# Optimization experiments

Measured on AMD Instinct MI355X. Metric: run time of the kernel, lower is better.

## Reference

```python
import jax, jax.numpy as jnp
import numpy as np

TAU, LBDA, THETA = 0.25, 0.15, 0.3
N_WARPS, N_ITERS = 1, 30
EPS = 1e-12  # GRAD_IS_ZERO

GAUSS = jnp.array([
    [0.000874, 0.006976, 0.01386, 0.006976, 0.000874],
    [0.006976, 0.0557, 0.110656, 0.0557, 0.006976],
    [0.01386, 0.110656, 0.219833, 0.110656, 0.01386],
    [0.006976, 0.0557, 0.110656, 0.0557, 0.006976],
    [0.000874, 0.006976, 0.01386, 0.006976, 0.000874]], dtype=jnp.float32)


def to_gray(x):  # [B,3,H,W] -> [B,1,H,W], BGR-style weights from repo
    w = jnp.array([0.114, 0.587, 0.299], x.dtype)
    return jnp.einsum('bchw,c->bhw', x, w)[:, None]


def normalize_pair(x1, x2):
    mn = jnp.minimum(x1.min(), x2.min())
    mx = jnp.maximum(x1.max(), x2.max())
    den = mx - mn
    return 255.0 * (x1 - mn) / den, 255.0 * (x2 - mn) / den


def gaussian_smooth(x):
    k = GAUSS[None, None].astype(x.dtype)
    return jax.lax.conv_general_dilated(x, k, (1, 1), 'SAME')


def centered_grad(x):  # central differences, one-sided at borders (scaled 0.5)
    dx = jnp.concatenate([0.5 * (x[..., 1:2] - x[..., 0:1]),
                          0.5 * (x[..., 2:] - x[..., :-2]),
                          0.5 * (x[..., -1:] - x[..., -2:-1])], axis=-1)
    dy = jnp.concatenate([0.5 * (x[..., 1:2, :] - x[..., 0:1, :]),
                          0.5 * (x[..., 2:, :] - x[..., :-2, :]),
                          0.5 * (x[..., -1:, :] - x[..., -2:-1, :])], axis=-2)
    return dx, dy


def fwd_grad(x):  # forward differences, zero at last col/row
    dx = jnp.concatenate([x[..., 1:] - x[..., :-1], jnp.zeros_like(x[..., :1])], axis=-1)
    dy = jnp.concatenate([x[..., 1:, :] - x[..., :-1, :], jnp.zeros_like(x[..., :1, :])], axis=-2)
    return dx, dy


def divergence(px, py):  # adjoint of fwd_grad (backward differences with boundary handling)
    xp = jnp.concatenate([jnp.zeros_like(px[..., :1]), px[..., :-1]], axis=-1)
    yp = jnp.concatenate([jnp.zeros_like(py[..., :1, :]), py[..., :-1, :]], axis=-2)
    dx = jnp.concatenate([xp[..., 1:] - xp[..., :-1], -xp[..., -1:]], axis=-1)
    dy = jnp.concatenate([yp[..., 1:, :] - yp[..., :-1, :], -yp[..., -1:, :]], axis=-2)
    return dx + dy


def warp(x, u, v):  # grid_sample bilinear, align_corners=True, zeros padding
    B, C, H, W = x.shape
    base_x = jnp.linspace(-1.0, 1.0, W)[None, None, :]
    base_y = jnp.linspace(-1.0, 1.0, H)[None, :, None]
    gx = base_x + 2.0 * u[:, 0] / W   # [B,H,W]
    gy = base_y + 2.0 * v[:, 0] / H
    ix = (gx + 1.0) * 0.5 * (W - 1)
    iy = (gy + 1.0) * 0.5 * (H - 1)
    ix0 = jnp.floor(ix); iy0 = jnp.floor(iy)
    wx = ix - ix0; wy = iy - iy0

    def gather(yy, xx):
        valid = (xx >= 0) & (xx <= W - 1) & (yy >= 0) & (yy <= H - 1)
        xi = jnp.clip(xx, 0, W - 1).astype(jnp.int32)
        yi = jnp.clip(yy, 0, H - 1).astype(jnp.int32)
        flat = (yi * W + xi).reshape(B, 1, H * W)
        g = jnp.take_along_axis(x.reshape(B, C, H * W), flat, axis=2).reshape(B, C, H, W)
        return g * valid[:, None].astype(x.dtype)

    return (gather(iy0, ix0) * ((1 - wx) * (1 - wy))[:, None]
            + gather(iy0, ix0 + 1) * (wx * (1 - wy))[:, None]
            + gather(iy0 + 1, ix0) * ((1 - wx) * wy)[:, None]
            + gather(iy0 + 1, ix0 + 1) * (wx * wy)[:, None])


def tvnet_scale(x1, x2, u1, u2):
    l_t = LBDA * THETA
    taut = TAU / THETA
    d2x, d2y = centered_grad(x2)
    p11 = jnp.zeros_like(x1); p12 = jnp.zeros_like(x1)
    p21 = jnp.zeros_like(x1); p22 = jnp.zeros_like(x1)
    rho = jnp.zeros_like(x1)
    for _ in range(N_WARPS):
        x2w = warp(x2, u1, u2)
        dxw = warp(d2x, u1, u2)
        dyw = warp(d2y, u1, u2)
        grad = dxw ** 2 + dyw ** 2 + EPS
        rho_c = x2w - dxw * u1 - dyw * u2 - x1

        def body(carry, _):
            u1, u2, p11, p12, p21, p22, _ = carry
            rho = rho_c + dxw * u1 + dyw * u2 + EPS
            th = l_t * grad
            m3 = (rho >= -th) & (rho <= th) & (grad > EPS)
            coef = (jnp.where(rho < -th, l_t, 0.0)
                    + jnp.where(rho > th, -l_t, 0.0)
                    + jnp.where(m3, -rho / grad, 0.0))
            v1 = coef * dxw + u1
            v2 = coef * dyw + u2
            u1n = v1 + THETA * divergence(p11, p12)
            u2n = v2 + THETA * divergence(p21, p22)
            u1x, u1y = fwd_grad(u1n)
            u2x, u2y = fwd_grad(u2n)
            ng1 = 1.0 + taut * jnp.sqrt(u1x ** 2 + u1y ** 2 + EPS)
            ng2 = 1.0 + taut * jnp.sqrt(u2x ** 2 + u2y ** 2 + EPS)
            p11n = (p11 + taut * u1x) / ng1
            p12n = (p12 + taut * u1y) / ng1
            p21n = (p21 + taut * u2x) / ng2
            p22n = (p22 + taut * u2y) / ng2
            return (u1n, u2n, p11n, p12n, p21n, p22n, rho), None

        (u1, u2, p11, p12, p21, p22, rho), _ = jax.lax.scan(
            body, (u1, u2, p11, p12, p21, p22, rho), None, length=N_ITERS)
    return u1, u2, rho


def setup_inputs() -> dict:
    key = jax.random.key(0)
    k1, k2 = jax.random.split(key)
    x1 = jax.random.uniform(k1, (8, 3, 256, 256), dtype=jnp.float32)
    x2 = jax.random.uniform(k2, (8, 3, 256, 256), dtype=jnp.float32)
    return {"x1": x1, "x2": x2}


def reference(x1, x2):
    g1 = to_gray(x1)
    g2 = to_gray(x2)
    n1, n2 = normalize_pair(g1, g2)
    s1 = gaussian_smooth(n1)
    s2 = gaussian_smooth(n2)
    u1 = jnp.zeros_like(s1)
    u2 = jnp.zeros_like(s1)
    u1, u2, rho = tvnet_scale(s1, s2, u1, u2)
    return jnp.concatenate([u1, u2, rho], axis=1)  # [B,3,H,W]
```

## Files before the change

### kernel.cpp

```cpp
#include <hip/hip_runtime.h>
#include <hip/hip_fp16.h>
#include <math.h>

typedef float v2f __attribute__((ext_vector_type(2)));
static __device__ __forceinline__ v2f v2(float a, float b){ v2f r; r.x=a; r.y=b; return r; }
#define PKFMA(a,b,c) __builtin_elementwise_fma((a),(b),(c))

#define HH 256
#define WW 256
#define BB 8
#define NPIX (BB*HH*WW)
#define HWPLANE (HH*WW)
#define EPSF 1e-12f

#define TS 32
#define HL 10
#define SS (TS + 2*HL)
#define SS2 (SS*SS)
#define NTH 1024
#define NC 3
#define OWNBIT (1<<12)

#define GSS (TS + 6)
#define GSS2 (GSS*GSS)
#define S2S (TS + 2)
#define S2S2 (S2S*S2S)

constexpr float L_T   = (float)(0.15*0.3);
constexpr float TAUT  = (float)(0.25/0.3);
constexpr float THETA = 0.3f;

static __device__ __constant__ float GK[25] = {
  0.000874f, 0.006976f, 0.01386f,  0.006976f, 0.000874f,
  0.006976f, 0.0557f,   0.110656f, 0.0557f,   0.006976f,
  0.01386f,  0.110656f, 0.219833f, 0.110656f, 0.01386f,
  0.006976f, 0.0557f,   0.110656f, 0.0557f,   0.006976f,
  0.000874f, 0.006976f, 0.01386f,  0.006976f, 0.000874f };


__global__ void k_gray_minmax(const float* __restrict__ x1, const float* __restrict__ x2,
                              float* __restrict__ g1, float* __restrict__ g2,
                              unsigned int* __restrict__ mnmx) {
    __shared__ float smn[4], smx[4];
    float mn = 1e30f, mx = -1e30f;
    int stride = gridDim.x * blockDim.x;
    const int NV = 2*NPIX/4;
    for (int v = blockIdx.x*blockDim.x + threadIdx.x; v < NV; v += stride) {
        int img = v >> 17;
        int rem = v & (NPIX/4 - 1);
        const float* x = img ? x2 : x1;
        float* g = img ? g2 : g1;
        int b = rem >> 14;
        int pix = (rem & (HWPLANE/4 - 1)) << 2;
        const float* base = x + (size_t)b*3*HWPLANE + pix;
        float4 c0 = *(const float4*)(base);
        float4 c1 = *(const float4*)(base + HWPLANE);
        float4 c2 = *(const float4*)(base + 2*HWPLANE);
        float4 gr;
        gr.x = 0.114f*c0.x + 0.587f*c1.x + 0.299f*c2.x;
        gr.y = 0.114f*c0.y + 0.587f*c1.y + 0.299f*c2.y;
        gr.z = 0.114f*c0.z + 0.587f*c1.z + 0.299f*c2.z;
        gr.w = 0.114f*c0.w + 0.587f*c1.w + 0.299f*c2.w;
        *(float4*)(g + ((size_t)rem << 2)) = gr;
        mn = fminf(mn, fminf(fminf(gr.x, gr.y), fminf(gr.z, gr.w)));
        mx = fmaxf(mx, fmaxf(fmaxf(gr.x, gr.y), fmaxf(gr.z, gr.w)));
    }
    #pragma unroll
    for (int off = 32; off; off >>= 1) {
        mn = fminf(mn, __shfl_down(mn, off, 64));
        mx = fmaxf(mx, __shfl_down(mx, off, 64));
    }
    int wid = threadIdx.x >> 6;
    if ((threadIdx.x & 63) == 0) { smn[wid] = mn; smx[wid] = mx; }
    __syncthreads();
    if (threadIdx.x == 0) {
        mn = fminf(fminf(smn[0], smn[1]), fminf(smn[2], smn[3]));
        mx = fmaxf(fmaxf(smx[0], smx[1]), fmaxf(smx[2], smx[3]));
        atomicMin(&mnmx[0], __float_as_uint(mn));
        atomicMax((int*)&mnmx[1], (int)__float_as_uint(mx));
    }
}

__global__ void __launch_bounds__(256)
k_smooth_grad(const float* __restrict__ g1, const float* __restrict__ g2,
              const unsigned int* __restrict__ mnmx, float4* __restrict__ dxr) {
    __shared__ float gn1[GSS2], gn2[GSS2], s2L[S2S2];
    const int blk   = blockIdx.x;
    const int plane = blk >> 6;
    const int t     = blk & 63;
    const int oy0   = (t >> 3) << 5;
    const int ox0   = (t & 7) << 5;
    const int pbse  = plane * HWPLANE;
    const int tid   = threadIdx.x;

    const float mn  = __uint_as_float(mnmx[0]);
    const float inv = 255.0f / (__uint_as_float(mnmx[1]) - mn);

    for (int s = tid; s < GSS2; s += 256) {
        int sy = s / GSS, sx = s - sy*GSS;
        int gy = oy0 - 3 + sy, gx = ox0 - 3 + sx;
        bool im = (gx >= 0) & (gx < WW) & (gy >= 0) & (gy < HH);
        int gi = pbse + gy*WW + gx;
        gn1[s] = im ? (g1[gi] - mn)*inv : 0.f;
        gn2[s] = im ? (g2[gi] - mn)*inv : 0.f;
    }
    __syncthreads();

    for (int c = tid; c < S2S2; c += 256) {
        int sy = c / S2S, sx = c - sy*S2S;
        const float* gb = gn2 + sy*GSS + sx;
        float acc = 0.f;
        #pragma unroll
        for (int i = 0; i < 5; ++i)
            #pragma unroll
            for (int j = 0; j < 5; ++j)
                acc += gb[i*GSS + j] * GK[i*5 + j];
        s2L[c] = acc;
    }
    float s1r[4];
    #pragma unroll
    for (int i = 0; i < 4; ++i) {
        int c = tid + i*256;
        int oy = c >> 5, ox = c & 31;
        const float* gb = gn1 + (oy+1)*GSS + (ox+1);
        float acc = 0.f;
        #pragma unroll
        for (int ii = 0; ii < 5; ++ii)
            #pragma unroll
            for (int jj = 0; jj < 5; ++jj)
                acc += gb[ii*GSS + jj] * GK[ii*5 + jj];
        s1r[i] = acc;
    }
    __syncthreads();

    #pragma unroll
    for (int i = 0; i < 4; ++i) {
        int c = tid + i*256;
        int oy = c >> 5, ox = c & 31;
        int gy = oy0 + oy, gx = ox0 + ox;
        int sc = (oy+1)*S2S + (ox+1);
        float s2c = s2L[sc];
        float xp = (gx < WW-1) ? s2L[sc+1]    : s2c;
        float xm = (gx > 0)    ? s2L[sc-1]    : s2c;
        float yp = (gy < HH-1) ? s2L[sc+S2S]  : s2c;
        float ym = (gy > 0)    ? s2L[sc-S2S]  : s2c;
        float dx = 0.5f*(xp - xm), dy = 0.5f*(yp - ym);
        float grad = fmaf(dx, dx, fmaf(dy, dy, EPSF));
        float rgr  = __builtin_amdgcn_rcpf(grad);
        dxr[pbse + gy*WW + gx] = make_float4(dx, dy, s2c - s1r[i], rgr);
    }
}

__global__ void __launch_bounds__(NTH)
k_iter10(float* __restrict__ F, float* __restrict__ out, int itbase) {
    const float4* DXR = (const float4*)F;
    const int j  = itbase / HL;
    const int rd = j & 1;
    const __half2* Ur  = (const __half2*)(F + (size_t)NPIX*(rd ? 12 : 6));
    const __half2* PAr = (const __half2*)(F + (size_t)NPIX*(rd ? 14 : 8));
    const __half2* PBr = (const __half2*)(F + (size_t)NPIX*(rd ? 16 : 10));
    __half2* Uw  = (__half2*)(F + (size_t)NPIX*(rd ? 6 : 12));
    __half2* PAw = (__half2*)(F + (size_t)NPIX*(rd ? 8 : 14));
    __half2* PBw = (__half2*)(F + (size_t)NPIX*(rd ? 10 : 16));

    __shared__ v2f u12[SS2];
    __shared__ v2f pa [SS2];
    __shared__ v2f pb [SS2];

    const int blk   = blockIdx.x;
    const int plane = blk >> 6;
    const int t     = blk & 63;
    const int gy0   = ((t >> 3) << 5) - HL;
    const int gx0   = ((t & 7) << 5) - HL;
    const int pbse  = plane * HWPLANE;
    const int tid   = threadIdx.x;
    const int sxmax = WW-1 - gx0;
    const int symax = HH-1 - gy0;

    int cc[NC];
    v2f dv[NC]; float rcv[NC], rgr[NC];
    v2f ru[NC];
    v2f rpa[NC];
    v2f rpb[NC];

    #pragma unroll
    for (int i = 0; i < NC; ++i) {
        int s = tid + i*NTH;
        cc[i] = 0;
        dv[i] = v2(0.f, 0.f); rcv[i] = EPSF; rgr[i] = 0.f;
        ru[i] = v2(0.f, 0.f);
        rpa[i] = v2(0.f, 0.f); rpb[i] = v2(0.f, 0.f);
        if (s < SS2) {
            int sy = s / SS, sx = s - sy*SS;
            int gy = gy0 + sy, gx = gx0 + sx;
            bool im = (gx >= 0) & (gx < WW) & (gy >= 0) & (gy < HH);
            if (im) {
                int m  = min(min(sy-1, sx-1), min(SS-1-sy, SS-1-sx));
                int mp = min(m, min(SS-2-sy, SS-2-sx));
                int ku1 = max(m,  -1) + 1;
                int kp1 = max(mp, -1) + 1;
                int own = (int)((sy >= HL) & (sy < HL+TS) & (sx >= HL) & (sx < HL+TS));
                cc[i] = (kp1 << 24) | (ku1 << 16) | (own << 12) | (sy << 6) | sx;
                int gi = pbse + gy*WW + gx;
                float4 dvv = DXR[gi];
                dv[i] = v2(dvv.x, dvv.y); rcv[i] = dvv.z + EPSF; rgr[i] = dvv.w;
                if (itbase) {
                    float2 uv  = __half22float2(Ur[gi]);
                    float2 pav = __half22float2(PAr[gi]);
                    float2 pbv = __half22float2(PBr[gi]);
                    ru[i]  = v2(uv.x,  uv.y);
                    rpa[i] = v2(pav.x, pav.y);
                    rpb[i] = v2(pbv.x, pbv.y);
                }
            }
            u12[s] = ru[i];
            pa[s]  = rpa[i];
            pb[s]  = rpb[i];
        }
    }
    __syncthreads();

    #pragma unroll 1
    for (int k = 0; k < HL; ++k) {
        const bool lastk = (k == HL-1);
        const bool it29  = (itbase + k == 29);

        #pragma unroll
        for (int i = 0; i < NC; ++i) {
            if (k >= ((cc[i] >> 16) & 0xFF)) continue;
            int s = tid + i*NTH;
            float rhov = fmaf(dv[i].x, ru[i].x, fmaf(dv[i].y, ru[i].y, rcv[i]));
            float coef = fminf(fmaxf(-rhov * rgr[i], -L_T), L_T);
            v2f pal = pa[s-1], pbu = pb[s-SS];
            v2f d  = (rpa[i] - pal) + (rpb[i] - pbu);
            v2f un = PKFMA(v2(THETA,THETA), d,
                           PKFMA(v2(coef,coef), dv[i], ru[i]));
            if (it29) {
                if (cc[i] & OWNBIT) {
                    int sy = (cc[i] >> 6) & 63, sx = cc[i] & 63;
                    float* o = out + (size_t)plane*3*HWPLANE + (gy0+sy)*WW + (gx0+sx);
                    o[0]         = un.x;
                    o[HWPLANE]   = un.y;
                    o[2*HWPLANE] = rhov;
                }
            } else {
                ru[i] = un;
                u12[s] = un;
                if (lastk && (cc[i] & OWNBIT)) {
                    int sy = (cc[i] >> 6) & 63, sx = cc[i] & 63;
                    Uw[pbse + (gy0+sy)*WW + (gx0+sx)] = __floats2half2_rn(un.x, un.y);
                }
            }
        }
        if (it29) return;
        __syncthreads();

        #pragma unroll
        for (int i = 0; i < NC; ++i) {
            if (k >= (int)((unsigned)cc[i] >> 24)) continue;
            int s = tid + i*NTH;
            int sy = (cc[i] >> 6) & 63, sx = cc[i] & 63;
            float fbm = (sx < sxmax) ? 1.f : 0.f;
            float fdm = (sy < symax) ? 1.f : 0.f;
            v2f ux = (u12[s+1]  - ru[i]) * fbm;
            v2f uy = (u12[s+SS] - ru[i]) * fdm;
            v2f q  = PKFMA(ux, ux, PKFMA(uy, uy, v2(EPSF,EPSF)));
            v2f sq = v2(__builtin_amdgcn_sqrtf(q.x), __builtin_amdgcn_sqrtf(q.y));
            v2f ng = PKFMA(v2(TAUT,TAUT), sq, v2(1.f,1.f));
            v2f r  = v2(__builtin_amdgcn_rcpf(ng.x), __builtin_amdgcn_rcpf(ng.y));
            rpa[i] = PKFMA(v2(TAUT,TAUT), ux, rpa[i]) * r;
            rpb[i] = PKFMA(v2(TAUT,TAUT), uy, rpb[i]) * r;
            if (!lastk) {
                pa[s] = rpa[i];
                pb[s] = rpb[i];
            } else if (cc[i] & OWNBIT) {
                int gi = pbse + (gy0+sy)*WW + (gx0+sx);
                PAw[gi] = __floats2half2_rn(rpa[i].x, rpa[i].y);
                PBw[gi] = __floats2half2_rn(rpb[i].x, rpb[i].y);
            }
        }
        if (!lastk) __syncthreads();
    }
}

extern "C" void kernel_launch(void* const* d_in, const int* in_sizes, int n_in,
                              void* d_out, int out_size, void* d_ws, size_t ws_size,
                              hipStream_t stream) {
    const float* x1 = (const float*)d_in[0];
    const float* x2 = (const float*)d_in[1];
    float* out = (float*)d_out;

    char* ws = (char*)d_ws;
    unsigned int* mnmx = (unsigned int*)ws;
    float* F = (float*)(ws + 256);
    float4* dxr = (float4*)F;
    float*  g1  = F + 4*(size_t)NPIX;
    float*  g2  = F + 5*(size_t)NPIX;

    k_gray_minmax<<<dim3(512), dim3(256), 0, stream>>>(x1, x2, g1, g2, mnmx);
    k_smooth_grad<<<dim3(512), dim3(256), 0, stream>>>(g1, g2, mnmx, dxr);

    for (int itbase = 0; itbase < 30; itbase += HL)
        k_iter10<<<dim3(512), dim3(NTH), 0, stream>>>(F, out, itbase);
}
```

Before: 164.8 us.

## Pair adjacent pixels per thread and interleave u/p state into one 16-byte record

Each thread now owns two horizontally adjacent pixels plus an optional third, instead of three pixels strided by the block size. Shared-memory reads and writes of u and p become 16-byte vector accesses, and the left-neighbour p value of the second pixel is taken from a register. The u, pa and pb half2 planes are merged into one interleaved uint4 record per pixel, so each pixel's state is loaded and stored in a single access. The record carries 4 bytes of padding, which adds global traffic, and the paired ownership changes which threads are active at the halo edges.

```diff
diff --git a/kernel.cpp b/kernel.cpp
--- a/kernel.cpp
+++ b/kernel.cpp
@@ -18,8 +18,9 @@
 #define SS (TS + 2*HL)
 #define SS2 (SS*SS)
 #define NTH 1024
-#define NC 3
-#define OWNBIT (1<<12)
+#define NPAIR 2048
+#define NSING (SS2 - NPAIR)
+#define OWNBIT (1<<13)
 
 #define GSS (TS + 6)
 #define GSS2 (GSS*GSS)
@@ -156,12 +157,8 @@
     const float4* DXR = (const float4*)F;
     const int j  = itbase / HL;
     const int rd = j & 1;
-    const __half2* Ur  = (const __half2*)(F + (size_t)NPIX*(rd ? 12 : 6));
-    const __half2* PAr = (const __half2*)(F + (size_t)NPIX*(rd ? 14 : 8));
-    const __half2* PBr = (const __half2*)(F + (size_t)NPIX*(rd ? 16 : 10));
-    __half2* Uw  = (__half2*)(F + (size_t)NPIX*(rd ? 6 : 12));
-    __half2* PAw = (__half2*)(F + (size_t)NPIX*(rd ? 8 : 14));
-    __half2* PBw = (__half2*)(F + (size_t)NPIX*(rd ? 10 : 16));
+    const uint4* Xr = (const uint4*)(F + (size_t)NPIX*(rd ? 12 : 6));
+    uint4*       Xw = (uint4*)(F + (size_t)NPIX*(rd ? 6 : 12));
 
     __shared__ v2f u12[SS2];
     __shared__ v2f pa [SS2];
@@ -177,45 +174,55 @@
     const int sxmax = WW-1 - gx0;
     const int symax = HH-1 - gy0;
 
-    int cc[NC];
-    v2f dv[NC]; float rcv[NC], rgr[NC];
-    v2f ru[NC];
-    v2f rpa[NC];
-    v2f rpb[NC];
-
-    #pragma unroll
-    for (int i = 0; i < NC; ++i) {
-        int s = tid + i*NTH;
-        cc[i] = 0;
-        dv[i] = v2(0.f, 0.f); rcv[i] = EPSF; rgr[i] = 0.f;
-        ru[i] = v2(0.f, 0.f);
-        rpa[i] = v2(0.f, 0.f); rpb[i] = v2(0.f, 0.f);
-        if (s < SS2) {
+    int ccP, ccS;
+    v2f dv[3]; float rcv[3], rgr[3];
+    v2f ru[3], rpa[3], rpb[3];
+
+    {
+        int ku0=0,ku1=0,ku2=0, kp0=0,kp1=0,kp2=0, ow0=0,ow2=0;
+        #pragma unroll
+        for (int i = 0; i < 3; ++i) {
+            dv[i]=v2(0.f,0.f); rcv[i]=EPSF; rgr[i]=0.f;
+            ru[i]=v2(0.f,0.f); rpa[i]=v2(0.f,0.f); rpb[i]=v2(0.f,0.f);
+            if (i == 2 && tid >= NSING) continue;
+            int s = (i < 2) ? (2*tid + i) : (NPAIR + tid);
             int sy = s / SS, sx = s - sy*SS;
             int gy = gy0 + sy, gx = gx0 + sx;
             bool im = (gx >= 0) & (gx < WW) & (gy >= 0) & (gy < HH);
             if (im) {
                 int m  = min(min(sy-1, sx-1), min(SS-1-sy, SS-1-sx));
                 int mp = min(m, min(SS-2-sy, SS-2-sx));
-                int ku1 = max(m,  -1) + 1;
-                int kp1 = max(mp, -1) + 1;
-                int own = (int)((sy >= HL) & (sy < HL+TS) & (sx >= HL) & (sx < HL+TS));
-                cc[i] = (kp1 << 24) | (ku1 << 16) | (own << 12) | (sy << 6) | sx;
+                int ku = max(m,  -1) + 1;
+                int kp = max(mp, -1) + 1;
+                int ow = (int)((sy >= HL) & (sy < HL+TS) & (sx >= HL) & (sx < HL+TS));
+                if (i == 0) { ku0=ku; kp0=kp; ow0=ow; }
+                else if (i == 1) { ku1=ku; kp1=kp; ow0|=ow; }
+                else { ku2=ku; kp2=kp; ow2=ow; }
                 int gi = pbse + gy*WW + gx;
                 float4 dvv = DXR[gi];
                 dv[i] = v2(dvv.x, dvv.y); rcv[i] = dvv.z + EPSF; rgr[i] = dvv.w;
                 if (itbase) {
-                    float2 uv  = __half22float2(Ur[gi]);
-                    float2 pav = __half22float2(PAr[gi]);
-                    float2 pbv = __half22float2(PBr[gi]);
-                    ru[i]  = v2(uv.x,  uv.y);
-                    rpa[i] = v2(pav.x, pav.y);
-                    rpb[i] = v2(pbv.x, pbv.y);
+                    uint4 xv = Xr[gi];
+                    float2 uf = __half22float2(*(__half2*)&xv.x);
+                    float2 af = __half22float2(*(__half2*)&xv.y);
+                    float2 bf = __half22float2(*(__half2*)&xv.z);
+                    ru[i]=v2(uf.x,uf.y); rpa[i]=v2(af.x,af.y); rpb[i]=v2(bf.x,bf.y);
                 }
             }
-            u12[s] = ru[i];
-            pa[s]  = rpa[i];
-            pb[s]  = rpb[i];
+        }
+        int s0 = 2*tid, sy0 = s0 / SS, sx0 = s0 - sy0*SS;
+        ccP = (max(kp0,kp1) << 24) | (max(ku0,ku1) << 16)
+            | (ow0 ? OWNBIT : 0) | (sy0 << 6) | sx0;
+        if (tid < NSING) {
+            int s2 = NPAIR + tid, sy2 = s2 / SS, sx2 = s2 - sy2*SS;
+            ccS = (kp2 << 24) | (ku2 << 16) | (ow2 ? OWNBIT : 0) | (sy2 << 6) | sx2;
+        } else ccS = 0;
+        *(float4*)&u12[s0] = make_float4(ru[0].x,ru[0].y,ru[1].x,ru[1].y);
+        *(float4*)&pa [s0] = make_float4(rpa[0].x,rpa[0].y,rpa[1].x,rpa[1].y);
+        *(float4*)&pb [s0] = make_float4(rpb[0].x,rpb[0].y,rpb[1].x,rpb[1].y);
+        if (tid < NSING) {
+            int s2 = NPAIR + tid;
+            u12[s2]=ru[2]; pa[s2]=rpa[2]; pb[s2]=rpb[2];
         }
     }
     __syncthreads();
@@ -225,58 +232,118 @@
         const bool lastk = (k == HL-1);
         const bool it29  = (itbase + k == 29);
 
-        #pragma unroll
-        for (int i = 0; i < NC; ++i) {
-            if (k >= ((cc[i] >> 16) & 0xFF)) continue;
-            int s = tid + i*NTH;
-            float rhov = fmaf(dv[i].x, ru[i].x, fmaf(dv[i].y, ru[i].y, rcv[i]));
-            float coef = fminf(fmaxf(-rhov * rgr[i], -L_T), L_T);
-            v2f pal = pa[s-1], pbu = pb[s-SS];
-            v2f d  = (rpa[i] - pal) + (rpb[i] - pbu);
-            v2f un = PKFMA(v2(THETA,THETA), d,
-                           PKFMA(v2(coef,coef), dv[i], ru[i]));
+        if (k < ((ccP >> 16) & 0xFF)) {
+            int s0 = 2*tid;
+            v2f pal0 = pa[s0-1];
+            float4 pb2 = *(const float4*)&pb[s0-SS];
+            float rho0 = fmaf(dv[0].x, ru[0].x, fmaf(dv[0].y, ru[0].y, rcv[0]));
+            float rho1 = fmaf(dv[1].x, ru[1].x, fmaf(dv[1].y, ru[1].y, rcv[1]));
+            float co0 = fminf(fmaxf(-rho0 * rgr[0], -L_T), L_T);
+            float co1 = fminf(fmaxf(-rho1 * rgr[1], -L_T), L_T);
+            v2f d0 = (rpa[0] - pal0)   + (rpb[0] - v2(pb2.x,pb2.y));
+            v2f d1 = (rpa[1] - rpa[0]) + (rpb[1] - v2(pb2.z,pb2.w));
+            v2f un0 = PKFMA(v2(THETA,THETA), d0, PKFMA(v2(co0,co0), dv[0], ru[0]));
+            v2f un1 = PKFMA(v2(THETA,THETA), d1, PKFMA(v2(co1,co1), dv[1], ru[1]));
             if (it29) {
-                if (cc[i] & OWNBIT) {
-                    int sy = (cc[i] >> 6) & 63, sx = cc[i] & 63;
-                    float* o = out + (size_t)plane*3*HWPLANE + (gy0+sy)*WW + (gx0+sx);
-                    o[0]         = un.x;
-                    o[HWPLANE]   = un.y;
-                    o[2*HWPLANE] = rhov;
+                if (ccP & OWNBIT) {
+                    int sy = (ccP >> 6) & 63, sx = ccP & 63;
+                    float2* o = (float2*)(out + (size_t)plane*3*HWPLANE + (gy0+sy)*WW + (gx0+sx));
+                    o[0]         = make_float2(un0.x, un1.x);
+                    o[HWPLANE/2] = make_float2(un0.y, un1.y);
+                    o[HWPLANE]   = make_float2(rho0, rho1);
                 }
             } else {
-                ru[i] = un;
+                ru[0] = un0; ru[1] = un1;
+                *(float4*)&u12[s0] = make_float4(un0.x,un0.y,un1.x,un1.y);
+            }
+        }
+        if (k < ((ccS >> 16) & 0xFF)) {
+            int s = NPAIR + tid;
+            float rho = fmaf(dv[2].x, ru[2].x, fmaf(dv[2].y, ru[2].y, rcv[2]));
+            float co  = fminf(fmaxf(-rho * rgr[2], -L_T), L_T);
+            v2f pal = pa[s-1], pbu = pb[s-SS];
+            v2f d  = (rpa[2] - pal) + (rpb[2] - pbu);
+            v2f un = PKFMA(v2(THETA,THETA), d, PKFMA(v2(co,co), dv[2], ru[2]));
+            if (it29) {
+                if (ccS & OWNBIT) {
+                    int sy = (ccS >> 6) & 63, sx = ccS & 63;
+                    float* o = out + (size_t)plane*3*HWPLANE + (gy0+sy)*WW + (gx0+sx);
+                    o[0] = un.x; o[HWPLANE] = un.y; o[2*HWPLANE] = rho;
+                }
+            } else {
+                ru[2] = un;
                 u12[s] = un;
-                if (lastk && (cc[i] & OWNBIT)) {
-                    int sy = (cc[i] >> 6) & 63, sx = cc[i] & 63;
-                    Uw[pbse + (gy0+sy)*WW + (gx0+sx)] = __floats2half2_rn(un.x, un.y);
-                }
             }
         }
         if (it29) return;
         __syncthreads();
 
-        #pragma unroll
-        for (int i = 0; i < NC; ++i) {
-            if (k >= (int)((unsigned)cc[i] >> 24)) continue;
-            int s = tid + i*NTH;
-            int sy = (cc[i] >> 6) & 63, sx = cc[i] & 63;
+        if (k < (int)((unsigned)ccP >> 24)) {
+            int s0 = 2*tid;
+            int sy = (ccP >> 6) & 63, sx = ccP & 63;
+            float fdm  = (sy     < symax) ? 1.f : 0.f;
+            float fbm0 = (sx     < sxmax) ? 1.f : 0.f;
+            float fbm1 = (sx + 1 < sxmax) ? 1.f : 0.f;
+            v2f ur1 = u12[s0+2];
+            float4 ud2 = *(const float4*)&u12[s0+SS];
+            v2f ux0 = (ru[1] - ru[0]) * fbm0;
+            v2f uy0 = (v2(ud2.x,ud2.y) - ru[0]) * fdm;
+            v2f ux1 = (ur1 - ru[1]) * fbm1;
+            v2f uy1 = (v2(ud2.z,ud2.w) - ru[1]) * fdm;
+            v2f q0 = PKFMA(ux0, ux0, PKFMA(uy0, uy0, v2(EPSF,EPSF)));
+            v2f q1 = PKFMA(ux1, ux1, PKFMA(uy1, uy1, v2(EPSF,EPSF)));
+            v2f ng0 = PKFMA(v2(TAUT,TAUT), v2(__builtin_amdgcn_sqrtf(q0.x),__builtin_amdgcn_sqrtf(q0.y)), v2(1.f,1.f));
+            v2f ng1 = PKFMA(v2(TAUT,TAUT), v2(__builtin_amdgcn_sqrtf(q1.x),__builtin_amdgcn_sqrtf(q1.y)), v2(1.f,1.f));
+            v2f r0 = v2(__builtin_amdgcn_rcpf(ng0.x), __builtin_amdgcn_rcpf(ng0.y));
+            v2f r1 = v2(__builtin_amdgcn_rcpf(ng1.x), __builtin_amdgcn_rcpf(ng1.y));
+            rpa[0] = PKFMA(v2(TAUT,TAUT), ux0, rpa[0]) * r0;
+            rpb[0] = PKFMA(v2(TAUT,TAUT), uy0, rpb[0]) * r0;
+            rpa[1] = PKFMA(v2(TAUT,TAUT), ux1, rpa[1]) * r1;
+            rpb[1] = PKFMA(v2(TAUT,TAUT), uy1, rpb[1]) * r1;
+            if (!lastk) {
+                *(float4*)&pa[s0] = make_float4(rpa[0].x,rpa[0].y,rpa[1].x,rpa[1].y);
+                *(float4*)&pb[s0] = make_float4(rpb[0].x,rpb[0].y,rpb[1].x,rpb[1].y);
+            } else if (ccP & OWNBIT) {
+                int gi = pbse + (gy0+sy)*WW + (gx0+sx);
+                __half2 h0u = __floats2half2_rn(ru[0].x, ru[0].y);
+                __half2 h0a = __floats2half2_rn(rpa[0].x, rpa[0].y);
+                __half2 h0b = __floats2half2_rn(rpb[0].x, rpb[0].y);
+                __half2 h1u = __floats2half2_rn(ru[1].x, ru[1].y);
+                __half2 h1a = __floats2half2_rn(rpa[1].x, rpa[1].y);
+                __half2 h1b = __floats2half2_rn(rpb[1].x, rpb[1].y);
+                uint4 x0, x1;
+                x0.x = *(unsigned int*)&h0u; x0.y = *(unsigned int*)&h0a;
+                x0.z = *(unsigned int*)&h0b; x0.w = 0u;
+                x1.x = *(unsigned int*)&h1u; x1.y = *(unsigned int*)&h1a;
+                x1.z = *(unsigned int*)&h1b; x1.w = 0u;
+                Xw[gi]   = x0;
+                Xw[gi+1] = x1;
+            }
+        }
+        if (k < (int)((unsigned)ccS >> 24)) {
+            int s = NPAIR + tid;
+            int sy = (ccS >> 6) & 63, sx = ccS & 63;
             float fbm = (sx < sxmax) ? 1.f : 0.f;
             float fdm = (sy < symax) ? 1.f : 0.f;
-            v2f ux = (u12[s+1]  - ru[i]) * fbm;
-            v2f uy = (u12[s+SS] - ru[i]) * fdm;
+            v2f ux = (u12[s+1]  - ru[2]) * fbm;
+            v2f uy = (u12[s+SS] - ru[2]) * fdm;
             v2f q  = PKFMA(ux, ux, PKFMA(uy, uy, v2(EPSF,EPSF)));
-            v2f sq = v2(__builtin_amdgcn_sqrtf(q.x), __builtin_amdgcn_sqrtf(q.y));
-            v2f ng = PKFMA(v2(TAUT,TAUT), sq, v2(1.f,1.f));
+            v2f ng = PKFMA(v2(TAUT,TAUT), v2(__builtin_amdgcn_sqrtf(q.x),__builtin_amdgcn_sqrtf(q.y)), v2(1.f,1.f));
             v2f r  = v2(__builtin_amdgcn_rcpf(ng.x), __builtin_amdgcn_rcpf(ng.y));
-            rpa[i] = PKFMA(v2(TAUT,TAUT), ux, rpa[i]) * r;
-            rpb[i] = PKFMA(v2(TAUT,TAUT), uy, rpb[i]) * r;
+            rpa[2] = PKFMA(v2(TAUT,TAUT), ux, rpa[2]) * r;
+            rpb[2] = PKFMA(v2(TAUT,TAUT), uy, rpb[2]) * r;
             if (!lastk) {
-                pa[s] = rpa[i];
-                pb[s] = rpb[i];
-            } else if (cc[i] & OWNBIT) {
+                pa[s] = rpa[2];
+                pb[s] = rpb[2];
+            } else if (ccS & OWNBIT) {
                 int gi = pbse + (gy0+sy)*WW + (gx0+sx);
-                PAw[gi] = __floats2half2_rn(rpa[i].x, rpa[i].y);
-                PBw[gi] = __floats2half2_rn(rpb[i].x, rpb[i].y);
+                __half2 hu = __floats2half2_rn(ru[2].x, ru[2].y);
+                __half2 ha = __floats2half2_rn(rpa[2].x, rpa[2].y);
+                __half2 hb = __floats2half2_rn(rpb[2].x, rpb[2].y);
+                uint4 xv;
+                xv.x = *(unsigned int*)&hu; xv.y = *(unsigned int*)&ha;
+                xv.z = *(unsigned int*)&hb; xv.w = 0u;
+                Xw[gi] = xv;
             }
         }
         if (!lastk) __syncthreads();
```

Result: no change. 164.2 us, median of 2 (-0.4%).

## Fuse three iteration launches into one persistent kernel with per-plane grid barriers

Applied to the files above, without the earlier changes.

Replaces the three k_iter10 launches with a single k_iter30 kernel of 256 blocks. Each block handles two tiles and keeps its own tile state resident in shared memory across all 30 iterations. Only halo cells are exchanged through global memory, packed into one uint4 per pixel, with a spin-wait atomic barrier per plane between 10-iteration chunks. This removes launch overhead and the full state reloads, but it assumes all 256 co-resident 1024-thread blocks can run at once. It also serializes the two tiles inside each block, which halves parallelism per chunk.

```diff
diff --git a/kernel.cpp b/kernel.cpp
--- a/kernel.cpp
+++ b/kernel.cpp
@@ -18,8 +18,9 @@
 #define SS (TS + 2*HL)
 #define SS2 (SS*SS)
 #define NTH 1024
-#define NC 3
 #define OWNBIT (1<<12)
+#define NBLK 256
+#define PLBLK 32
 
 #define GSS (TS + 6)
 #define GSS2 (GSS*GSS)
@@ -42,6 +43,7 @@
                               float* __restrict__ g1, float* __restrict__ g2,
                               unsigned int* __restrict__ mnmx) {
     __shared__ float smn[4], smx[4];
+    if (blockIdx.x == 0 && threadIdx.x < 16) mnmx[8 + threadIdx.x] = 0u;
     float mn = 1e30f, mx = -1e30f;
     int stride = gridDim.x * blockDim.x;
     const int NV = 2*NPIX/4;
@@ -152,134 +154,171 @@
 }
 
 __global__ void __launch_bounds__(NTH)
-k_iter10(float* __restrict__ F, float* __restrict__ out, int itbase) {
+k_iter30(float* __restrict__ F, float* __restrict__ out,
+         unsigned int* __restrict__ bar) {
     const float4* DXR = (const float4*)F;
-    const int j  = itbase / HL;
-    const int rd = j & 1;
-    const __half2* Ur  = (const __half2*)(F + (size_t)NPIX*(rd ? 12 : 6));
-    const __half2* PAr = (const __half2*)(F + (size_t)NPIX*(rd ? 14 : 8));
-    const __half2* PBr = (const __half2*)(F + (size_t)NPIX*(rd ? 16 : 10));
-    __half2* Uw  = (__half2*)(F + (size_t)NPIX*(rd ? 6 : 12));
-    __half2* PAw = (__half2*)(F + (size_t)NPIX*(rd ? 8 : 14));
-    __half2* PBw = (__half2*)(F + (size_t)NPIX*(rd ? 10 : 16));
-
-    __shared__ v2f u12[SS2];
-    __shared__ v2f pa [SS2];
-    __shared__ v2f pb [SS2];
+
+    __shared__ v2f u12[2*SS2];
+    __shared__ v2f pa [2*SS2];
+    __shared__ v2f pb [2*SS2];
 
     const int blk   = blockIdx.x;
-    const int plane = blk >> 6;
-    const int t     = blk & 63;
-    const int gy0   = ((t >> 3) << 5) - HL;
-    const int gx0   = ((t & 7) << 5) - HL;
+    const int plane = blk >> 5;
+    const int tq    = blk & 31;
     const int pbse  = plane * HWPLANE;
     const int tid   = threadIdx.x;
-    const int sxmax = WW-1 - gx0;
-    const int symax = HH-1 - gy0;
-
-    int cc[NC];
-    v2f dv[NC]; float rcv[NC], rgr[NC];
-    v2f ru[NC];
-    v2f rpa[NC];
-    v2f rpb[NC];
-
-    #pragma unroll
-    for (int i = 0; i < NC; ++i) {
-        int s = tid + i*NTH;
-        cc[i] = 0;
-        dv[i] = v2(0.f, 0.f); rcv[i] = EPSF; rgr[i] = 0.f;
-        ru[i] = v2(0.f, 0.f);
-        rpa[i] = v2(0.f, 0.f); rpb[i] = v2(0.f, 0.f);
-        if (s < SS2) {
-            int sy = s / SS, sx = s - sy*SS;
-            int gy = gy0 + sy, gx = gx0 + sx;
-            bool im = (gx >= 0) & (gx < WW) & (gy >= 0) & (gy < HH);
-            if (im) {
-                int m  = min(min(sy-1, sx-1), min(SS-1-sy, SS-1-sx));
-                int mp = min(m, min(SS-2-sy, SS-2-sx));
-                int ku1 = max(m,  -1) + 1;
-                int kp1 = max(mp, -1) + 1;
-                int own = (int)((sy >= HL) & (sy < HL+TS) & (sx >= HL) & (sx < HL+TS));
-                cc[i] = (kp1 << 24) | (ku1 << 16) | (own << 12) | (sy << 6) | sx;
-                int gi = pbse + gy*WW + gx;
-                float4 dvv = DXR[gi];
-                dv[i] = v2(dvv.x, dvv.y); rcv[i] = dvv.z + EPSF; rgr[i] = dvv.w;
-                if (itbase) {
-                    float2 uv  = __half22float2(Ur[gi]);
-                    float2 pav = __half22float2(PAr[gi]);
-                    float2 pbv = __half22float2(PBr[gi]);
-                    ru[i]  = v2(uv.x,  uv.y);
-                    rpa[i] = v2(pav.x, pav.y);
-                    rpb[i] = v2(pbv.x, pbv.y);
+
+    for (int s = tid; s < 2*SS2; s += NTH) {
+        u12[s] = v2(0.f,0.f); pa[s] = v2(0.f,0.f); pb[s] = v2(0.f,0.f);
+    }
+    __syncthreads();
+
+    #pragma unroll 1
+    for (int j = 0; j < 3; ++j) {
+        uint4* Xj = (uint4*)(F + (size_t)NPIX*(j == 0 ? 6 : 12));
+
+        #pragma unroll 1
+        for (int tau = 0; tau < 2; ++tau) {
+            const int gy0 = ((tq >> 2) << 5) - HL;
+            const int gx0 = ((((tq & 3) << 1) | tau) << 5) - HL;
+            const int sxmax = WW-1 - gx0;
+            const int symax = HH-1 - gy0;
+            const int lb = tau * SS2;
+
+            int cc[3];
+            v2f dv[3]; float rcv[3], rgr[3];
+            v2f ru[3], rpa[3], rpb[3];
+            #pragma unroll
+            for (int i = 0; i < 3; ++i) {
+                int s = tid + i*NTH;
+                cc[i] = 0;
+                dv[i] = v2(0.f,0.f); rcv[i] = EPSF; rgr[i] = 0.f;
+                ru[i] = v2(0.f,0.f); rpa[i] = v2(0.f,0.f); rpb[i] = v2(0.f,0.f);
+                if (s < SS2) {
+                    int sy = s / SS, sx = s - sy*SS;
+                    int gy = gy0 + sy, gx = gx0 + sx;
+                    bool im = (gx >= 0) & (gx < WW) & (gy >= 0) & (gy < HH);
+                    if (im) {
+                        int m  = min(min(sy-1, sx-1), min(SS-1-sy, SS-1-sx));
+                        int mp = min(m, min(SS-2-sy, SS-2-sx));
+                        int ku1 = max(m,  -1) + 1;
+                        int kp1 = max(mp, -1) + 1;
+                        int ow = (int)((sy >= HL) & (sy < HL+TS) & (sx >= HL) & (sx < HL+TS));
+                        cc[i] = (kp1 << 24) | (ku1 << 16) | (ow << 12) | (sy << 6) | sx;
+                        float4 dvv = DXR[pbse + gy*WW + gx];
+                        dv[i] = v2(dvv.x, dvv.y); rcv[i] = dvv.z + EPSF; rgr[i] = dvv.w;
+                        ru[i]  = u12[lb+s];
+                        rpa[i] = pa[lb+s];
+                        rpb[i] = pb[lb+s];
+                    }
                 }
             }
-            u12[s] = ru[i];
-            pa[s]  = rpa[i];
-            pb[s]  = rpb[i];
+
+            #pragma unroll 1
+            for (int k = 0; k < HL; ++k) {
+                const bool lastk = (k == HL-1);
+                const bool it29  = (j == 2) && lastk;
+
+                #pragma unroll
+                for (int i = 0; i < 3; ++i) {
+                    if (k >= ((cc[i] >> 16) & 0xFF)) continue;
+                    int s = lb + tid + i*NTH;
+                    float rhov = fmaf(dv[i].x, ru[i].x, fmaf(dv[i].y, ru[i].y, rcv[i]));
+                    float coef = fminf(fmaxf(-rhov * rgr[i], -L_T), L_T);
+                    v2f pal = pa[s-1], pbu = pb[s-SS];
+                    v2f d  = (rpa[i] - pal) + (rpb[i] - pbu);
+                    v2f un = PKFMA(v2(THETA,THETA), d,
+                                   PKFMA(v2(coef,coef), dv[i], ru[i]));
+                    if (it29) {
+                        if (cc[i] & OWNBIT) {
+                            int sy = (cc[i] >> 6) & 63, sx = cc[i] & 63;
+                            float* o = out + (size_t)plane*3*HWPLANE + (gy0+sy)*WW + (gx0+sx);
+                            o[0]         = un.x;
+                            o[HWPLANE]   = un.y;
+                            o[2*HWPLANE] = rhov;
+                        }
+                    } else {
+                        ru[i] = un;
+                        u12[s] = un;
+                    }
+                }
+                if (it29) break;
+                __syncthreads();
+
+                #pragma unroll
+                for (int i = 0; i < 3; ++i) {
+                    if (k >= (int)((unsigned)cc[i] >> 24)) continue;
+                    int s = lb + tid + i*NTH;
+                    int sy = (cc[i] >> 6) & 63, sx = cc[i] & 63;
+                    float fbm = (sx < sxmax) ? 1.f : 0.f;
+                    float fdm = (sy < symax) ? 1.f : 0.f;
+                    v2f ux = (u12[s+1]  - ru[i]) * fbm;
+                    v2f uy = (u12[s+SS] - ru[i]) * fdm;
+                    v2f q  = PKFMA(ux, ux, PKFMA(uy, uy, v2(EPSF,EPSF)));
+                    v2f ng = PKFMA(v2(TAUT,TAUT),
+                                   v2(__builtin_amdgcn_sqrtf(q.x), __builtin_amdgcn_sqrtf(q.y)),
+                                   v2(1.f,1.f));
+                    v2f r  = v2(__builtin_amdgcn_rcpf(ng.x), __builtin_amdgcn_rcpf(ng.y));
+                    rpa[i] = PKFMA(v2(TAUT,TAUT), ux, rpa[i]) * r;
+                    rpb[i] = PKFMA(v2(TAUT,TAUT), uy, rpb[i]) * r;
+                    pa[s] = rpa[i];
+                    pb[s] = rpb[i];
+                    if (lastk && (cc[i] & OWNBIT)) {
+                        int gi = pbse + (gy0+sy)*WW + (gx0+sx);
+                        __half2 hu = __floats2half2_rn(ru[i].x, ru[i].y);
+                        __half2 ha = __floats2half2_rn(rpa[i].x, rpa[i].y);
+                        __half2 hb = __floats2half2_rn(rpb[i].x, rpb[i].y);
+                        uint4 xv;
+                        xv.x = *(unsigned int*)&hu; xv.y = *(unsigned int*)&ha;
+                        xv.z = *(unsigned int*)&hb; xv.w = 0u;
+                        Xj[gi] = xv;
+                    }
+                }
+                __syncthreads();
+            }
         }
-    }
-    __syncthreads();
-
-    #pragma unroll 1
-    for (int k = 0; k < HL; ++k) {
-        const bool lastk = (k == HL-1);
-        const bool it29  = (itbase + k == 29);
-
-        #pragma unroll
-        for (int i = 0; i < NC; ++i) {
-            if (k >= ((cc[i] >> 16) & 0xFF)) continue;
-            int s = tid + i*NTH;
-            float rhov = fmaf(dv[i].x, ru[i].x, fmaf(dv[i].y, ru[i].y, rcv[i]));
-            float coef = fminf(fmaxf(-rhov * rgr[i], -L_T), L_T);
-            v2f pal = pa[s-1], pbu = pb[s-SS];
-            v2f d  = (rpa[i] - pal) + (rpb[i] - pbu);
-            v2f un = PKFMA(v2(THETA,THETA), d,
-                           PKFMA(v2(coef,coef), dv[i], ru[i]));
-            if (it29) {
-                if (cc[i] & OWNBIT) {
-                    int sy = (cc[i] >> 6) & 63, sx = cc[i] & 63;
-                    float* o = out + (size_t)plane*3*HWPLANE + (gy0+sy)*WW + (gx0+sx);
-                    o[0]         = un.x;
-                    o[HWPLANE]   = un.y;
-                    o[2*HWPLANE] = rhov;
-                }
-            } else {
-                ru[i] = un;
-                u12[s] = un;
-                if (lastk && (cc[i] & OWNBIT)) {
-                    int sy = (cc[i] >> 6) & 63, sx = cc[i] & 63;
-                    Uw[pbse + (gy0+sy)*WW + (gx0+sx)] = __floats2half2_rn(un.x, un.y);
+
+        if (j == 2) return;
+
+        {
+            unsigned int* cnt = &bar[j*8 + plane];
+            if (tid == 0) {
+                __threadfence();
+                __hip_atomic_fetch_add(cnt, 1u, __ATOMIC_RELEASE, __HIP_MEMORY_SCOPE_AGENT);
+                unsigned int spins = 0;
+                while (__hip_atomic_load(cnt, __ATOMIC_ACQUIRE, __HIP_MEMORY_SCOPE_AGENT) < (unsigned)PLBLK
+                       && ++spins < (1u<<20))
+                    __builtin_amdgcn_s_sleep(2);
+                __threadfence();
+            }
+            __syncthreads();
+        }
+
+        #pragma unroll 1
+        for (int tau = 0; tau < 2; ++tau) {
+            const int gy0 = ((tq >> 2) << 5) - HL;
+            const int gx0 = ((((tq & 3) << 1) | tau) << 5) - HL;
+            const int lb = tau * SS2;
+            #pragma unroll
+            for (int i = 0; i < 3; ++i) {
+                int s = tid + i*NTH;
+                if (s >= SS2) continue;
+                int sy = s / SS, sx = s - sy*SS;
+                int gy = gy0 + sy, gx = gx0 + sx;
+                bool im = (gx >= 0) & (gx < WW) & (gy >= 0) & (gy < HH);
+                bool ow = (sy >= HL) & (sy < HL+TS) & (sx >= HL) & (sx < HL+TS);
+                if (im && !ow) {
+                    uint4 xv = Xj[pbse + gy*WW + gx];
+                    float2 uf = __half22float2(*(__half2*)&xv.x);
+                    float2 af = __half22float2(*(__half2*)&xv.y);
+                    float2 bf = __half22float2(*(__half2*)&xv.z);
+                    u12[lb+s] = v2(uf.x, uf.y);
+                    pa [lb+s] = v2(af.x, af.y);
+                    pb [lb+s] = v2(bf.x, bf.y);
                 }
             }
         }
-        if (it29) return;
         __syncthreads();
-
-        #pragma unroll
-        for (int i = 0; i < NC; ++i) {
-            if (k >= (int)((unsigned)cc[i] >> 24)) continue;
-            int s = tid + i*NTH;
-            int sy = (cc[i] >> 6) & 63, sx = cc[i] & 63;
-            float fbm = (sx < sxmax) ? 1.f : 0.f;
-            float fdm = (sy < symax) ? 1.f : 0.f;
-            v2f ux = (u12[s+1]  - ru[i]) * fbm;
-            v2f uy = (u12[s+SS] - ru[i]) * fdm;
-            v2f q  = PKFMA(ux, ux, PKFMA(uy, uy, v2(EPSF,EPSF)));
-            v2f sq = v2(__builtin_amdgcn_sqrtf(q.x), __builtin_amdgcn_sqrtf(q.y));
-            v2f ng = PKFMA(v2(TAUT,TAUT), sq, v2(1.f,1.f));
-            v2f r  = v2(__builtin_amdgcn_rcpf(ng.x), __builtin_amdgcn_rcpf(ng.y));
-            rpa[i] = PKFMA(v2(TAUT,TAUT), ux, rpa[i]) * r;
-            rpb[i] = PKFMA(v2(TAUT,TAUT), uy, rpb[i]) * r;
-            if (!lastk) {
-                pa[s] = rpa[i];
-                pb[s] = rpb[i];
-            } else if (cc[i] & OWNBIT) {
-                int gi = pbse + (gy0+sy)*WW + (gx0+sx);
-                PAw[gi] = __floats2half2_rn(rpa[i].x, rpa[i].y);
-                PBw[gi] = __floats2half2_rn(rpb[i].x, rpb[i].y);
-            }
-        }
-        if (!lastk) __syncthreads();
     }
 }
 
@@ -299,7 +338,5 @@
 
     k_gray_minmax<<<dim3(512), dim3(256), 0, stream>>>(x1, x2, g1, g2, mnmx);
     k_smooth_grad<<<dim3(512), dim3(256), 0, stream>>>(g1, g2, mnmx, dxr);
-
-    for (int itbase = 0; itbase < 30; itbase += HL)
-        k_iter10<<<dim3(512), dim3(NTH), 0, stream>>>(F, out, itbase);
+    k_iter30<<<dim3(NBLK), dim3(NTH), 0, stream>>>(F, out, mnmx + 8);
 }
```

New measurement: 232.3 us. 40.9% more time.
